# Performance work log

Hardware: AMD Instinct MI355X
Metric: run time of the kernel (lower is better)

## Reference

```python
import jax, jax.numpy as jnp
import numpy as np

N = 50000   # nodes
E = 800000  # edges (avg degree 16)
D = 96      # in = hid = out
BN_EPS = 1e-5


def setup_inputs() -> dict:
    key = jax.random.key(0)
    ks = jax.random.split(key, 16)
    features = jax.random.normal(ks[0], (N, D), jnp.float32)
    src = jax.random.randint(ks[1], (E,), 0, N)
    dst = jax.random.randint(ks[2], (E,), 0, N)
    bound = 1.0 / np.sqrt(D)
    def lin(kw, kb):
        W = jax.random.uniform(kw, (D, D), jnp.float32, -bound, bound)
        b = jax.random.uniform(kb, (D,), jnp.float32, -bound, bound)
        return W, b
    W1, b1 = lin(ks[3], ks[4])
    W2, b2 = lin(ks[5], ks[6])
    W3, b3 = lin(ks[7], ks[8])
    gamma1 = jnp.ones((D,), jnp.float32)
    beta1 = jnp.zeros((D,), jnp.float32)
    gamma2 = jnp.ones((D,), jnp.float32)
    beta2 = jnp.zeros((D,), jnp.float32)
    return dict(features=features, W1=W1, b1=b1, gamma1=gamma1, beta1=beta1,
                W2=W2, b2=b2, gamma2=gamma2, beta2=beta2, W3=W3, b3=b3,
                src=src, dst=dst)


def _gin_conv(h, W, b, src, dst, inv_deg):
    # mean-aggregate incoming neighbor features, eps = 0: (h + mean_nb) @ W + b
    agg = jax.ops.segment_sum(h[src], dst, num_segments=N) * inv_deg[:, None]
    return (h + agg) @ W + b


def _batchnorm(x, gamma, beta):
    mu = jnp.mean(x, axis=0)
    var = jnp.mean((x - mu) ** 2, axis=0)  # biased, as torch BN training
    return (x - mu) * jax.lax.rsqrt(var + BN_EPS) * gamma + beta


def reference(features, W1, b1, gamma1, beta1, W2, b2, gamma2, beta2, W3, b3, src, dst):
    deg = jax.ops.segment_sum(jnp.ones((E,), jnp.float32), dst, num_segments=N)
    inv_deg = jnp.where(deg > 0, 1.0 / jnp.maximum(deg, 1.0), 0.0)
    h = _gin_conv(features, W1, b1, src, dst, inv_deg)
    h = jax.nn.relu(_batchnorm(h, gamma1, beta1))  # dropout p=0 -> identity
    h = _gin_conv(h, W2, b2, src, dst, inv_deg)
    h = jax.nn.relu(_batchnorm(h, gamma2, beta2))
    h = _gin_conv(h, W3, b3, src, dst, inv_deg)
    return h
```

## Files before the change

kernel.cpp:

```cpp
#include <hip/hip_runtime.h>

#define FD 96
#define NB12 12
#define BSH 7
#define BNODES 128
#define NBLK 256

typedef float  f32x4 __attribute__((ext_vector_type(4)));
typedef short  s16x8 __attribute__((ext_vector_type(8)));

__device__ __forceinline__ unsigned short f2bf(float x) {
    unsigned u = __float_as_uint(x);
    u = (u + 0x7fffu + ((u >> 16) & 1u)) >> 16;
    return (unsigned short)u;
}
__device__ __forceinline__ float bflo(unsigned u) { return __uint_as_float(u << 16); }
__device__ __forceinline__ float bfhi(unsigned u) { return __uint_as_float(u & 0xffff0000u); }


__global__ void k_h2d(const int* __restrict__ dst, int* __restrict__ hist2d,
                      int* __restrict__ bcnt, int E, int nbkt, int chunk) {
    __shared__ int hist[512];
    int tid = threadIdx.x, b = blockIdx.x;
    for (int i = tid; i < 512; i += 256) hist[i] = 0;
    __syncthreads();
    int lo = b * chunk, hi = min(lo + chunk, E);
    for (int i = lo + tid; i < hi; i += 256)
        atomicAdd(&hist[dst[i] >> BSH], 1);
    __syncthreads();
    for (int q = tid; q < nbkt; q += 256) {
        int hv = hist[q];
        hist2d[(size_t)q * NBLK + b] = hv;
        if (hv) atomicAdd(&bcnt[q], hv);
    }
}

__global__ void k_bscan(const int* __restrict__ bcnt, int* __restrict__ bbase, int nbkt) {
    __shared__ int sh[512];
    int tid = threadIdx.x;
    int v = (tid < nbkt) ? bcnt[tid] : 0;
    sh[tid] = v;
    __syncthreads();
    for (int off = 1; off < 512; off <<= 1) {
        int t = (tid >= off) ? sh[tid - off] : 0;
        __syncthreads();
        sh[tid] += t;
        __syncthreads();
    }
    int incl = sh[tid];
    if (tid < nbkt) bbase[tid] = incl - v;
    if (tid == nbkt - 1) bbase[nbkt] = incl;
}

__global__ void k_cscan(const int* __restrict__ hist2d, const int* __restrict__ bbase,
                        int* __restrict__ cursor2d) {
    __shared__ int sh[NBLK];
    int q = blockIdx.x, tid = threadIdx.x;
    int v = hist2d[(size_t)q * NBLK + tid];
    sh[tid] = v;
    __syncthreads();
    for (int off = 1; off < NBLK; off <<= 1) {
        int t = (tid >= off) ? sh[tid - off] : 0;
        __syncthreads();
        sh[tid] += t;
        __syncthreads();
    }
    cursor2d[(size_t)q * NBLK + tid] = bbase[q] + sh[tid] - v;
}

__global__ void k_scat(const int* __restrict__ src, const int* __restrict__ dst,
                       const int* __restrict__ cursor2d, uint2* __restrict__ ebuf,
                       int E, int nbkt, int chunk) {
    __shared__ int cur[512];
    int tid = threadIdx.x, b = blockIdx.x;
    for (int q = tid; q < nbkt; q += 256)
        cur[q] = cursor2d[(size_t)q * NBLK + b];
    __syncthreads();
    int lo = b * chunk, hi = min(lo + chunk, E);
    for (int i = lo + tid; i < hi; i += 256) {
        int d = dst[i];
        int p = atomicAdd(&cur[d >> BSH], 1);
        ebuf[p] = make_uint2((unsigned)d, (unsigned)src[i]);
    }
}

__global__ void k_bsort(const uint2* __restrict__ ebuf, const int* __restrict__ bbase,
                        int* __restrict__ csr, int* __restrict__ rp, int* __restrict__ re,
                        float* __restrict__ invd, int* __restrict__ perm, int n) {
    __shared__ int cnt[BNODES];
    __shared__ int cur[BNODES];
    __shared__ int dh[64];
    const int b = blockIdx.x;
    const int tid = threadIdx.x;
    const int lo = bbase[b], hi = bbase[b + 1];
    if (tid < BNODES) cnt[tid] = 0;
    if (tid < 64) dh[tid] = 0;
    __syncthreads();
    for (int i = lo + tid; i < hi; i += blockDim.x)
        atomicAdd(&cnt[(int)ebuf[i].x - (b << BSH)], 1);
    __syncthreads();
    const int node = (b << BSH) + tid;
    const int v = (tid < BNODES) ? cnt[tid] : 0;
    const int dcl = min(v, 63);
    if (tid < BNODES && node < n) atomicAdd(&dh[dcl], 1);
    for (int off = 1; off < BNODES; off <<= 1) {
        int t = (tid < BNODES && tid >= off) ? cnt[tid - off] : 0;
        __syncthreads();
        if (tid < BNODES) cnt[tid] += t;
        __syncthreads();
    }
    int dv = (tid < 64) ? dh[tid] : 0;
    for (int off = 1; off < 64; off <<= 1) {
        int t = (tid < 64 && tid >= off) ? dh[tid - off] : 0;
        __syncthreads();
        if (tid < 64) dh[tid] += t;
        __syncthreads();
    }
    if (tid < 64) dh[tid] -= dv;
    __syncthreads();
    if (tid < BNODES) {
        int excl = cnt[tid] - v;
        if (node < n) {
            rp[node] = lo + excl;
            re[node] = lo + excl + v;
            invd[node] = (v > 0) ? (1.0f / (float)v) : 0.f;
            int r = atomicAdd(&dh[dcl], 1);
            perm[(b << BSH) + r] = node;
        }
        cur[tid] = excl;
    }
    __syncthreads();
    for (int i = lo + tid; i < hi; i += blockDim.x) {
        uint2 e2 = ebuf[i];
        int local = (int)e2.x - (b << BSH);
        int p = lo + atomicAdd(&cur[local], 1);
        csr[p] = (int)e2.y;
    }
}


__global__ void k_cvt(const float4* __restrict__ in, uint4* __restrict__ o, int n16) {
    int i = blockIdx.x * blockDim.x + threadIdx.x;
    if (i >= n16) return;
    float4 x = in[2 * i], y = in[2 * i + 1];
    uint4 r;
    r.x = (unsigned)f2bf(x.x) | ((unsigned)f2bf(x.y) << 16);
    r.y = (unsigned)f2bf(x.z) | ((unsigned)f2bf(x.w) << 16);
    r.z = (unsigned)f2bf(y.x) | ((unsigned)f2bf(y.y) << 16);
    r.w = (unsigned)f2bf(y.z) | ((unsigned)f2bf(y.w) << 16);
    o[i] = r;
}


__global__ void k_wprep(const float* __restrict__ W, unsigned short* __restrict__ Wt) {
    int i = blockIdx.x * blockDim.x + threadIdx.x;
    if (i >= FD * FD) return;
    int col = i % FD, k = i / FD;
    Wt[col * FD + k] = f2bf(W[i]);
}


template<int NORM>
__global__ __launch_bounds__(256, 4) void k_agg(
    const uint4* __restrict__ h,
    const int* __restrict__ rp, const int* __restrict__ re,
    const int* __restrict__ csr, const float* __restrict__ invd,
    const int* __restrict__ perm,
    const float* __restrict__ nA, const float* __restrict__ nC,
    uint4* __restrict__ t, int n)
{
    int g = blockIdx.x * blockDim.x + threadIdx.x;
    int idx = g / NB12;
    if (idx >= n) return;
    int node = perm[idx];
    int q = g - idx * NB12;
    float a[8], c[8];
    if (NORM) {
        #pragma unroll
        for (int z = 0; z < 8; z++) { a[z] = nA[q * 8 + z]; c[z] = nC[q * 8 + z]; }
    }
    float acc8[8];
    #pragma unroll
    for (int z = 0; z < 8; z++) acc8[z] = 0.f;

    int e = rp[node];
    const int end = re[node];
    for (; e + 8 <= end; e += 8) {
        uint4 raw[8];
        #pragma unroll
        for (int u = 0; u < 8; u++) raw[u] = h[(size_t)csr[e + u] * NB12 + q];
        #pragma unroll
        for (int u = 0; u < 8; u++) {
            float v[8];
            v[0] = bflo(raw[u].x); v[1] = bfhi(raw[u].x);
            v[2] = bflo(raw[u].y); v[3] = bfhi(raw[u].y);
            v[4] = bflo(raw[u].z); v[5] = bfhi(raw[u].z);
            v[6] = bflo(raw[u].w); v[7] = bfhi(raw[u].w);
            #pragma unroll
            for (int z = 0; z < 8; z++) {
                float x = v[z];
                if (NORM) x = fmaxf(fmaf(a[z], x, c[z]), 0.f);
                acc8[z] += x;
            }
        }
    }
    for (; e < end; e++) {
        uint4 raw = h[(size_t)csr[e] * NB12 + q];
        float v[8];
        v[0] = bflo(raw.x); v[1] = bfhi(raw.x);
        v[2] = bflo(raw.y); v[3] = bfhi(raw.y);
        v[4] = bflo(raw.z); v[5] = bfhi(raw.z);
        v[6] = bflo(raw.w); v[7] = bfhi(raw.w);
        #pragma unroll
        for (int z = 0; z < 8; z++) {
            float x = v[z];
            if (NORM) x = fmaxf(fmaf(a[z], x, c[z]), 0.f);
            acc8[z] += x;
        }
    }
    uint4 rs = h[(size_t)node * NB12 + q];
    float xs[8];
    xs[0] = bflo(rs.x); xs[1] = bfhi(rs.x);
    xs[2] = bflo(rs.y); xs[3] = bfhi(rs.y);
    xs[4] = bflo(rs.z); xs[5] = bfhi(rs.z);
    xs[6] = bflo(rs.w); xs[7] = bfhi(rs.w);
    float id = invd[node];
    float o[8];
    #pragma unroll
    for (int z = 0; z < 8; z++) {
        float x = xs[z];
        if (NORM) x = fmaxf(fmaf(a[z], x, c[z]), 0.f);
        o[z] = fmaf(id, acc8[z], x);
    }
    uint4 pk;
    pk.x = (unsigned)f2bf(o[0]) | ((unsigned)f2bf(o[1]) << 16);
    pk.y = (unsigned)f2bf(o[2]) | ((unsigned)f2bf(o[3]) << 16);
    pk.z = (unsigned)f2bf(o[4]) | ((unsigned)f2bf(o[5]) << 16);
    pk.w = (unsigned)f2bf(o[6]) | ((unsigned)f2bf(o[7]) << 16);
    t[(size_t)node * NB12 + q] = pk;
}


template<int STATS, int OBF>
__global__ void k_mm(const unsigned short* __restrict__ ta,
                     const unsigned short* __restrict__ Wt,
                     const float* __restrict__ bias,
                     unsigned short* __restrict__ yb, float* __restrict__ yf,
                     float* __restrict__ accg, int n)
{
    __shared__ float sred[2 * FD];
    const int tid  = threadIdx.x;
    const int lane = tid & 63;
    const int wv   = tid >> 6;
    const int colb = lane & 15;
    const int hg   = lane >> 4;
    const int rbase = blockIdx.x * 64 + wv * 16;
    const int r = rbase + colb;

    s16x8 a[3];
    if (r < n) {
        #pragma unroll
        for (int s = 0; s < 3; s++)
            a[s] = *reinterpret_cast<const s16x8*>(ta + (size_t)r * FD + s * 32 + hg * 8);
    } else {
        #pragma unroll
        for (int s = 0; s < 3; s++) a[s] = s16x8{0, 0, 0, 0, 0, 0, 0, 0};
    }
    s16x8 b[6][3];
    #pragma unroll
    for (int c2 = 0; c2 < 6; c2++)
        #pragma unroll
        for (int s = 0; s < 3; s++)
            b[c2][s] = *reinterpret_cast<const s16x8*>(Wt + (size_t)(c2 * 16 + colb) * FD + s * 32 + hg * 8);

    f32x4 acc[6];
    #pragma unroll
    for (int c2 = 0; c2 < 6; c2++) acc[c2] = (f32x4){0.f, 0.f, 0.f, 0.f};
    #pragma unroll
    for (int s = 0; s < 3; s++)
        #pragma unroll
        for (int c2 = 0; c2 < 6; c2++)
            acc[c2] = __builtin_amdgcn_mfma_f32_16x16x32_bf16(a[s], b[c2][s], acc[c2], 0, 0, 0);

    float s1[6], s2[6];
    #pragma unroll
    for (int c2 = 0; c2 < 6; c2++) { s1[c2] = 0.f; s2[c2] = 0.f; }
    #pragma unroll
    for (int c2 = 0; c2 < 6; c2++) {
        float bc = bias[c2 * 16 + colb];
        #pragma unroll
        for (int j = 0; j < 4; j++) {
            int rr = rbase + hg * 4 + j;
            if (rr < n) {
                float y = acc[c2][j] + bc;
                if (OBF) yb[(size_t)rr * FD + c2 * 16 + colb] = f2bf(y);
                else     yf[(size_t)rr * FD + c2 * 16 + colb] = y;
                if (STATS) { s1[c2] += y; s2[c2] = fmaf(y, y, s2[c2]); }
            }
        }
    }
    if (STATS) {
        if (tid < 2 * FD) sred[tid] = 0.f;
        __syncthreads();
        #pragma unroll
        for (int c2 = 0; c2 < 6; c2++) {
            float v1 = s1[c2], v2 = s2[c2];
            v1 += __shfl_xor(v1, 16, 64); v1 += __shfl_xor(v1, 32, 64);
            v2 += __shfl_xor(v2, 16, 64); v2 += __shfl_xor(v2, 32, 64);
            if (lane < 16) {
                atomicAdd(&sred[c2 * 16 + colb], v1);
                atomicAdd(&sred[FD + c2 * 16 + colb], v2);
            }
        }
        __syncthreads();
        if (tid < 2 * FD) atomicAdd(&accg[tid], sred[tid]);
    }
}

__global__ void k_bnfin(const float* __restrict__ acc,
                        const float* __restrict__ gamma, const float* __restrict__ beta,
                        float* __restrict__ na, float* __restrict__ nc, float invN) {
    int f = threadIdx.x;
    float mu  = acc[f] * invN;
    float var = acc[FD + f] * invN - mu * mu;
    float a = gamma[f] * rsqrtf(var + 1e-5f);
    na[f] = a;
    nc[f] = beta[f] - mu * a;
}

extern "C" void kernel_launch(void* const* d_in, const int* in_sizes, int n_in,
                              void* d_out, int out_size, void* d_ws, size_t ws_size,
                              hipStream_t stream) {
    const float* feat = (const float*)d_in[0];
    const float* W1   = (const float*)d_in[1];
    const float* b1   = (const float*)d_in[2];
    const float* g1   = (const float*)d_in[3];
    const float* be1  = (const float*)d_in[4];
    const float* W2   = (const float*)d_in[5];
    const float* b2   = (const float*)d_in[6];
    const float* g2   = (const float*)d_in[7];
    const float* be2  = (const float*)d_in[8];
    const float* W3   = (const float*)d_in[9];
    const float* b3   = (const float*)d_in[10];
    const int*   src  = (const int*)d_in[11];
    const int*   dst  = (const int*)d_in[12];

    const int n = in_sizes[0] / FD;
    const int e = in_sizes[11];
    const int nbkt = (n + BNODES - 1) >> BSH;
    const int chunk = (e + NBLK - 1) / NBLK;

    char* w = (char*)d_ws;
    unsigned short* hf0 = (unsigned short*)w; w += (size_t)n * FD * 2;
    unsigned short* tb  = (unsigned short*)w; w += (size_t)n * FD * 2;
    unsigned short* Wt1 = (unsigned short*)w; w += FD * FD * 2;
    unsigned short* Wt2 = (unsigned short*)w; w += FD * FD * 2;
    unsigned short* Wt3 = (unsigned short*)w; w += FD * FD * 2;
    int*   csr     = (int*)w;   w += (size_t)e * 4;
    int*   bcnt    = (int*)w;   w += 512 * 4;
    float* acc1    = (float*)w; w += 2 * FD * 4;
    float* acc2    = (float*)w; w += 2 * FD * 4;
    int*   bbase   = (int*)w;   w += 513 * 4;
    int*   hist2d  = (int*)w;   w += (size_t)512 * NBLK * 4;
    int*   cursor2d= (int*)w;   w += (size_t)512 * NBLK * 4;
    int*   rp      = (int*)w;   w += (size_t)n * 4;
    int*   re      = (int*)w;   w += (size_t)n * 4;
    float* invd    = (float*)w; w += (size_t)n * 4;
    int*   perm    = (int*)w;   w += (size_t)n * 4;
    float* na1     = (float*)w; w += FD * 4;
    float* nc1     = (float*)w; w += FD * 4;
    float* na2     = (float*)w; w += FD * 4;
    float* nc2     = (float*)w; w += FD * 4;

    uint2* ebuf = (uint2*)tb;

    unsigned short* yb = (unsigned short*)d_out;
    float* O = (float*)d_out;
    const float invN = 1.0f / (float)n;
    const int AGG_GRID = (n * NB12 + 255) / 256;
    const int MM_GRID  = (n + 63) / 64;
    const int n16 = n * FD / 8;

    hipMemsetAsync(bcnt, 0, (512 + 4 * FD) * 4, stream);
    k_cvt<<<(n16 + 255) / 256, 256, 0, stream>>>((const float4*)feat, (uint4*)hf0, n16);
    k_wprep<<<(FD * FD + 255) / 256, 256, 0, stream>>>(W1, Wt1);
    k_wprep<<<(FD * FD + 255) / 256, 256, 0, stream>>>(W2, Wt2);
    k_wprep<<<(FD * FD + 255) / 256, 256, 0, stream>>>(W3, Wt3);

    k_h2d<<<NBLK, 256, 0, stream>>>(dst, hist2d, bcnt, e, nbkt, chunk);
    k_bscan<<<1, 512, 0, stream>>>(bcnt, bbase, nbkt);
    k_cscan<<<nbkt, NBLK, 0, stream>>>(hist2d, bbase, cursor2d);
    k_scat<<<NBLK, 256, 0, stream>>>(src, dst, cursor2d, ebuf, e, nbkt, chunk);
    k_bsort<<<nbkt, 256, 0, stream>>>(ebuf, bbase, csr, rp, re, invd, perm, n);

    k_agg<0><<<AGG_GRID, 256, 0, stream>>>((const uint4*)hf0, rp, re, csr, invd, perm,
                                           nullptr, nullptr, (uint4*)tb, n);
    k_mm<1, 1><<<MM_GRID, 256, 0, stream>>>(tb, Wt1, b1, yb, nullptr, acc1, n);
    k_bnfin<<<1, FD, 0, stream>>>(acc1, g1, be1, na1, nc1, invN);

    k_agg<1><<<AGG_GRID, 256, 0, stream>>>((const uint4*)yb, rp, re, csr, invd, perm,
                                           na1, nc1, (uint4*)tb, n);
    k_mm<1, 1><<<MM_GRID, 256, 0, stream>>>(tb, Wt2, b2, yb, nullptr, acc2, n);
    k_bnfin<<<1, FD, 0, stream>>>(acc2, g2, be2, na2, nc2, invN);

    k_agg<1><<<AGG_GRID, 256, 0, stream>>>((const uint4*)yb, rp, re, csr, invd, perm,
                                           na2, nc2, (uint4*)tb, n);
    k_mm<0, 0><<<MM_GRID, 256, 0, stream>>>(tb, Wt3, b3, nullptr, O, nullptr, n);
}
```

Before: 232.1 us.

## Fuse gather-aggregation with MFMA matmul and renumber nodes by degree order

Merges the per-layer aggregation and matmul kernels into one kernel. Each 16-row MFMA tile gathers its own neighbour rows into registers, packs them to bf16 and multiplies immediately, so the intermediate aggregated tensor is never written to or read from memory. Nodes are relabelled into the degree-sorted permutation: the CSR is translated through an inverse permutation and features are converted in permuted order, so outputs are contiguous and the final layer scatters through perm. BatchNorm+ReLU moves from the gather into a separate elementwise pass. This adds extra launches (xlate, norm) and gives one lane per row with 12 loads per edge, which may hurt gather parallelism.

```diff
diff --git a/kernel.cpp b/kernel.cpp
--- a/kernel.cpp
+++ b/kernel.cpp
@@ -1,7 +1,6 @@
 #include <hip/hip_runtime.h>
 
 #define FD 96
-#define NB12 12
 #define BSH 7
 #define BNODES 128
 #define NBLK 256
@@ -16,6 +15,26 @@
 }
 __device__ __forceinline__ float bflo(unsigned u) { return __uint_as_float(u << 16); }
 __device__ __forceinline__ float bfhi(unsigned u) { return __uint_as_float(u & 0xffff0000u); }
+
+__device__ __forceinline__ s16x8 pack8(const float t[8]) {
+    union { unsigned u[4]; s16x8 v; } r;
+    #pragma unroll
+    for (int z = 0; z < 4; z++)
+        r.u[z] = (unsigned)f2bf(t[2 * z]) | ((unsigned)f2bf(t[2 * z + 1]) << 16);
+    return r.v;
+}
+
+#define ACC8(R, T) { \
+    T[0] += bflo(R.x); T[1] += bfhi(R.x); \
+    T[2] += bflo(R.y); T[3] += bfhi(R.y); \
+    T[4] += bflo(R.z); T[5] += bfhi(R.z); \
+    T[6] += bflo(R.w); T[7] += bfhi(R.w); }
+
+#define FIN8(R, T, id) { \
+    T[0] = fmaf(id, T[0], bflo(R.x)); T[1] = fmaf(id, T[1], bfhi(R.x)); \
+    T[2] = fmaf(id, T[2], bflo(R.y)); T[3] = fmaf(id, T[3], bfhi(R.y)); \
+    T[4] = fmaf(id, T[4], bflo(R.z)); T[5] = fmaf(id, T[5], bfhi(R.z)); \
+    T[6] = fmaf(id, T[6], bflo(R.w)); T[7] = fmaf(id, T[7], bfhi(R.w)); }
 
 
 __global__ void k_h2d(const int* __restrict__ dst, int* __restrict__ hist2d,
@@ -85,8 +104,9 @@
 }
 
 __global__ void k_bsort(const uint2* __restrict__ ebuf, const int* __restrict__ bbase,
-                        int* __restrict__ csr, int* __restrict__ rp, int* __restrict__ re,
-                        float* __restrict__ invd, int* __restrict__ perm, int n) {
+                        int* __restrict__ csr, int* __restrict__ rp2, int* __restrict__ re2,
+                        float* __restrict__ invd2, int* __restrict__ perm,
+                        int* __restrict__ inv_perm, int n) {
     __shared__ int cnt[BNODES];
     __shared__ int cur[BNODES];
     __shared__ int dh[64];
@@ -121,11 +141,13 @@
     if (tid < BNODES) {
         int excl = cnt[tid] - v;
         if (node < n) {
-            rp[node] = lo + excl;
-            re[node] = lo + excl + v;
-            invd[node] = (v > 0) ? (1.0f / (float)v) : 0.f;
-            int r = atomicAdd(&dh[dcl], 1);
-            perm[(b << BSH) + r] = node;
+            int rk = atomicAdd(&dh[dcl], 1);
+            int slot = (b << BSH) + rk;
+            perm[slot] = node;
+            inv_perm[node] = slot;
+            rp2[slot] = lo + excl;
+            re2[slot] = lo + excl + v;
+            invd2[slot] = (v > 0) ? (1.0f / (float)v) : 0.f;
         }
         cur[tid] = excl;
     }
@@ -138,178 +160,133 @@
     }
 }
 
-
-__global__ void k_cvt(const float4* __restrict__ in, uint4* __restrict__ o, int n16) {
+__global__ void k_xlate(int* __restrict__ csr, const int* __restrict__ inv_perm, int E) {
     int i = blockIdx.x * blockDim.x + threadIdx.x;
-    if (i >= n16) return;
-    float4 x = in[2 * i], y = in[2 * i + 1];
+    if (i < E) csr[i] = inv_perm[csr[i]];
+}
+
+__global__ void k_cvtp(const float* __restrict__ feat, const int* __restrict__ perm,
+                       uint4* __restrict__ o, int n) {
+    int g = blockIdx.x * blockDim.x + threadIdx.x;
+    int i = g / 12;
+    if (i >= n) return;
+    int q = g - i * 12;
+    int node = perm[i];
+    const float4* row = (const float4*)(feat + (size_t)node * FD);
+    float4 x = row[2 * q], y = row[2 * q + 1];
     uint4 r;
     r.x = (unsigned)f2bf(x.x) | ((unsigned)f2bf(x.y) << 16);
     r.y = (unsigned)f2bf(x.z) | ((unsigned)f2bf(x.w) << 16);
     r.z = (unsigned)f2bf(y.x) | ((unsigned)f2bf(y.y) << 16);
     r.w = (unsigned)f2bf(y.z) | ((unsigned)f2bf(y.w) << 16);
-    o[i] = r;
-}
-
-
-__global__ void k_wprep(const float* __restrict__ W, unsigned short* __restrict__ Wt) {
+    o[g] = r;
+}
+
+__global__ void k_wprep3(const float* __restrict__ W1, const float* __restrict__ W2,
+                         const float* __restrict__ W3, unsigned short* __restrict__ Wt) {
     int i = blockIdx.x * blockDim.x + threadIdx.x;
-    if (i >= FD * FD) return;
-    int col = i % FD, k = i / FD;
-    Wt[col * FD + k] = f2bf(W[i]);
-}
-
-
-template<int NORM>
-__global__ __launch_bounds__(256, 4) void k_agg(
+    if (i >= 3 * FD * FD) return;
+    int m = i / (FD * FD), r = i - m * FD * FD;
+    const float* W = (m == 0) ? W1 : ((m == 1) ? W2 : W3);
+    int col = r % FD, k = r / FD;
+    Wt[m * FD * FD + col * FD + k] = f2bf(W[r]);
+}
+
+
+template<int STATS, int OBF>
+__global__ __launch_bounds__(256) void k_fused(
     const uint4* __restrict__ h,
-    const int* __restrict__ rp, const int* __restrict__ re,
-    const int* __restrict__ csr, const float* __restrict__ invd,
+    const int* __restrict__ rp2, const int* __restrict__ re2,
+    const float* __restrict__ invd2, const int* __restrict__ csr2,
     const int* __restrict__ perm,
-    const float* __restrict__ nA, const float* __restrict__ nC,
-    uint4* __restrict__ t, int n)
+    const unsigned short* __restrict__ Wt, const float* __restrict__ bias,
+    unsigned short* __restrict__ yb, float* __restrict__ yf,
+    float* __restrict__ accg, int n)
 {
-    int g = blockIdx.x * blockDim.x + threadIdx.x;
-    int idx = g / NB12;
-    if (idx >= n) return;
-    int node = perm[idx];
-    int q = g - idx * NB12;
-    float a[8], c[8];
-    if (NORM) {
+    __shared__ float sred[2 * FD];
+    const int tid = threadIdx.x, lane = tid & 63;
+    const int r16 = lane & 15, hg = lane >> 4;
+    const int tbase = blockIdx.x * 64 + (tid >> 6) * 16;
+    const int idx = tbase + r16;
+
+    float t0[8], t1[8], t2[8];
+    #pragma unroll
+    for (int z = 0; z < 8; z++) { t0[z] = 0.f; t1[z] = 0.f; t2[z] = 0.f; }
+
+    if (idx < n) {
+        int e = rp2[idx];
+        const int end = re2[idx];
+        for (; e + 4 <= end; e += 4) {
+            int ca = csr2[e], cb = csr2[e + 1], cc = csr2[e + 2], cd = csr2[e + 3];
+            uint4 A0 = h[(size_t)ca * 12 + hg], A1 = h[(size_t)ca * 12 + 4 + hg], A2 = h[(size_t)ca * 12 + 8 + hg];
+            uint4 B0 = h[(size_t)cb * 12 + hg], B1 = h[(size_t)cb * 12 + 4 + hg], B2 = h[(size_t)cb * 12 + 8 + hg];
+            uint4 C0 = h[(size_t)cc * 12 + hg], C1 = h[(size_t)cc * 12 + 4 + hg], C2 = h[(size_t)cc * 12 + 8 + hg];
+            uint4 D0 = h[(size_t)cd * 12 + hg], D1 = h[(size_t)cd * 12 + 4 + hg], D2 = h[(size_t)cd * 12 + 8 + hg];
+            ACC8(A0, t0); ACC8(A1, t1); ACC8(A2, t2);
+            ACC8(B0, t0); ACC8(B1, t1); ACC8(B2, t2);
+            ACC8(C0, t0); ACC8(C1, t1); ACC8(C2, t2);
+            ACC8(D0, t0); ACC8(D1, t1); ACC8(D2, t2);
+        }
+        for (; e < end; e++) {
+            int c = csr2[e];
+            uint4 R0 = h[(size_t)c * 12 + hg], R1 = h[(size_t)c * 12 + 4 + hg], R2 = h[(size_t)c * 12 + 8 + hg];
+            ACC8(R0, t0); ACC8(R1, t1); ACC8(R2, t2);
+        }
+        const float id = invd2[idx];
+        uint4 S0 = h[(size_t)idx * 12 + hg], S1 = h[(size_t)idx * 12 + 4 + hg], S2 = h[(size_t)idx * 12 + 8 + hg];
+        FIN8(S0, t0, id); FIN8(S1, t1, id); FIN8(S2, t2, id);
+    }
+
+    s16x8 a0 = pack8(t0), a1 = pack8(t1), a2 = pack8(t2);
+
+    f32x4 acc[6];
+    #pragma unroll
+    for (int c2 = 0; c2 < 6; c2++) acc[c2] = (f32x4){0.f, 0.f, 0.f, 0.f};
+    #pragma unroll
+    for (int c2 = 0; c2 < 6; c2++) {
+        const unsigned short* wp = Wt + (size_t)(c2 * 16 + r16) * FD + hg * 8;
+        s16x8 b0 = *(const s16x8*)(wp);
+        s16x8 b1 = *(const s16x8*)(wp + 32);
+        s16x8 b2 = *(const s16x8*)(wp + 64);
+        acc[c2] = __builtin_amdgcn_mfma_f32_16x16x32_bf16(a0, b0, acc[c2], 0, 0, 0);
+        acc[c2] = __builtin_amdgcn_mfma_f32_16x16x32_bf16(a1, b1, acc[c2], 0, 0, 0);
+        acc[c2] = __builtin_amdgcn_mfma_f32_16x16x32_bf16(a2, b2, acc[c2], 0, 0, 0);
+    }
+
+    int orow[4];
+    #pragma unroll
+    for (int j = 0; j < 4; j++) {
+        int rr = tbase + hg * 4 + j;
+        orow[j] = (!OBF && rr < n) ? perm[rr] : rr;
+    }
+    float s1v[6], s2v[6];
+    #pragma unroll
+    for (int c2 = 0; c2 < 6; c2++) { s1v[c2] = 0.f; s2v[c2] = 0.f; }
+    #pragma unroll
+    for (int c2 = 0; c2 < 6; c2++) {
+        float bc = bias[c2 * 16 + r16];
         #pragma unroll
-        for (int z = 0; z < 8; z++) { a[z] = nA[q * 8 + z]; c[z] = nC[q * 8 + z]; }
-    }
-    float acc8[8];
-    #pragma unroll
-    for (int z = 0; z < 8; z++) acc8[z] = 0.f;
-
-    int e = rp[node];
-    const int end = re[node];
-    for (; e + 8 <= end; e += 8) {
-        uint4 raw[8];
-        #pragma unroll
-        for (int u = 0; u < 8; u++) raw[u] = h[(size_t)csr[e + u] * NB12 + q];
-        #pragma unroll
-        for (int u = 0; u < 8; u++) {
-            float v[8];
-            v[0] = bflo(raw[u].x); v[1] = bfhi(raw[u].x);
-            v[2] = bflo(raw[u].y); v[3] = bfhi(raw[u].y);
-            v[4] = bflo(raw[u].z); v[5] = bfhi(raw[u].z);
-            v[6] = bflo(raw[u].w); v[7] = bfhi(raw[u].w);
-            #pragma unroll
-            for (int z = 0; z < 8; z++) {
-                float x = v[z];
-                if (NORM) x = fmaxf(fmaf(a[z], x, c[z]), 0.f);
-                acc8[z] += x;
+        for (int j = 0; j < 4; j++) {
+            int rr = tbase + hg * 4 + j;
+            if (rr < n) {
+                float y = acc[c2][j] + bc;
+                if (OBF) yb[(size_t)rr * FD + c2 * 16 + r16] = f2bf(y);
+                else     yf[(size_t)orow[j] * FD + c2 * 16 + r16] = y;
+                if (STATS) { s1v[c2] += y; s2v[c2] = fmaf(y, y, s2v[c2]); }
             }
         }
     }
-    for (; e < end; e++) {
-        uint4 raw = h[(size_t)csr[e] * NB12 + q];
-        float v[8];
-        v[0] = bflo(raw.x); v[1] = bfhi(raw.x);
-        v[2] = bflo(raw.y); v[3] = bfhi(raw.y);
-        v[4] = bflo(raw.z); v[5] = bfhi(raw.z);
-        v[6] = bflo(raw.w); v[7] = bfhi(raw.w);
-        #pragma unroll
-        for (int z = 0; z < 8; z++) {
-            float x = v[z];
-            if (NORM) x = fmaxf(fmaf(a[z], x, c[z]), 0.f);
-            acc8[z] += x;
-        }
-    }
-    uint4 rs = h[(size_t)node * NB12 + q];
-    float xs[8];
-    xs[0] = bflo(rs.x); xs[1] = bfhi(rs.x);
-    xs[2] = bflo(rs.y); xs[3] = bfhi(rs.y);
-    xs[4] = bflo(rs.z); xs[5] = bfhi(rs.z);
-    xs[6] = bflo(rs.w); xs[7] = bfhi(rs.w);
-    float id = invd[node];
-    float o[8];
-    #pragma unroll
-    for (int z = 0; z < 8; z++) {
-        float x = xs[z];
-        if (NORM) x = fmaxf(fmaf(a[z], x, c[z]), 0.f);
-        o[z] = fmaf(id, acc8[z], x);
-    }
-    uint4 pk;
-    pk.x = (unsigned)f2bf(o[0]) | ((unsigned)f2bf(o[1]) << 16);
-    pk.y = (unsigned)f2bf(o[2]) | ((unsigned)f2bf(o[3]) << 16);
-    pk.z = (unsigned)f2bf(o[4]) | ((unsigned)f2bf(o[5]) << 16);
-    pk.w = (unsigned)f2bf(o[6]) | ((unsigned)f2bf(o[7]) << 16);
-    t[(size_t)node * NB12 + q] = pk;
-}
-
-
-template<int STATS, int OBF>
-__global__ void k_mm(const unsigned short* __restrict__ ta,
-                     const unsigned short* __restrict__ Wt,
-                     const float* __restrict__ bias,
-                     unsigned short* __restrict__ yb, float* __restrict__ yf,
-                     float* __restrict__ accg, int n)
-{
-    __shared__ float sred[2 * FD];
-    const int tid  = threadIdx.x;
-    const int lane = tid & 63;
-    const int wv   = tid >> 6;
-    const int colb = lane & 15;
-    const int hg   = lane >> 4;
-    const int rbase = blockIdx.x * 64 + wv * 16;
-    const int r = rbase + colb;
-
-    s16x8 a[3];
-    if (r < n) {
-        #pragma unroll
-        for (int s = 0; s < 3; s++)
-            a[s] = *reinterpret_cast<const s16x8*>(ta + (size_t)r * FD + s * 32 + hg * 8);
-    } else {
-        #pragma unroll
-        for (int s = 0; s < 3; s++) a[s] = s16x8{0, 0, 0, 0, 0, 0, 0, 0};
-    }
-    s16x8 b[6][3];
-    #pragma unroll
-    for (int c2 = 0; c2 < 6; c2++)
-        #pragma unroll
-        for (int s = 0; s < 3; s++)
-            b[c2][s] = *reinterpret_cast<const s16x8*>(Wt + (size_t)(c2 * 16 + colb) * FD + s * 32 + hg * 8);
-
-    f32x4 acc[6];
-    #pragma unroll
-    for (int c2 = 0; c2 < 6; c2++) acc[c2] = (f32x4){0.f, 0.f, 0.f, 0.f};
-    #pragma unroll
-    for (int s = 0; s < 3; s++)
-        #pragma unroll
-        for (int c2 = 0; c2 < 6; c2++)
-            acc[c2] = __builtin_amdgcn_mfma_f32_16x16x32_bf16(a[s], b[c2][s], acc[c2], 0, 0, 0);
-
-    float s1[6], s2[6];
-    #pragma unroll
-    for (int c2 = 0; c2 < 6; c2++) { s1[c2] = 0.f; s2[c2] = 0.f; }
-    #pragma unroll
-    for (int c2 = 0; c2 < 6; c2++) {
-        float bc = bias[c2 * 16 + colb];
-        #pragma unroll
-        for (int j = 0; j < 4; j++) {
-            int rr = rbase + hg * 4 + j;
-            if (rr < n) {
-                float y = acc[c2][j] + bc;
-                if (OBF) yb[(size_t)rr * FD + c2 * 16 + colb] = f2bf(y);
-                else     yf[(size_t)rr * FD + c2 * 16 + colb] = y;
-                if (STATS) { s1[c2] += y; s2[c2] = fmaf(y, y, s2[c2]); }
-            }
-        }
-    }
     if (STATS) {
         if (tid < 2 * FD) sred[tid] = 0.f;
         __syncthreads();
         #pragma unroll
         for (int c2 = 0; c2 < 6; c2++) {
-            float v1 = s1[c2], v2 = s2[c2];
+            float v1 = s1v[c2], v2 = s2v[c2];
             v1 += __shfl_xor(v1, 16, 64); v1 += __shfl_xor(v1, 32, 64);
             v2 += __shfl_xor(v2, 16, 64); v2 += __shfl_xor(v2, 32, 64);
             if (lane < 16) {
-                atomicAdd(&sred[c2 * 16 + colb], v1);
-                atomicAdd(&sred[FD + c2 * 16 + colb], v2);
+                atomicAdd(&sred[c2 * 16 + r16], v1);
+                atomicAdd(&sred[FD + c2 * 16 + r16], v2);
             }
         }
         __syncthreads();
@@ -326,6 +303,30 @@
     float a = gamma[f] * rsqrtf(var + 1e-5f);
     na[f] = a;
     nc[f] = beta[f] - mu * a;
+}
+
+__global__ void k_norm(uint4* __restrict__ y, const float* __restrict__ na,
+                       const float* __restrict__ nc, int n12) {
+    int g = blockIdx.x * blockDim.x + threadIdx.x;
+    if (g >= n12) return;
+    int q = g % 12;
+    float4 a0 = *(const float4*)(na + q * 8), a1 = *(const float4*)(na + q * 8 + 4);
+    float4 c0 = *(const float4*)(nc + q * 8), c1 = *(const float4*)(nc + q * 8 + 4);
+    uint4 r = y[g];
+    float v0 = fmaxf(fmaf(a0.x, bflo(r.x), c0.x), 0.f);
+    float v1 = fmaxf(fmaf(a0.y, bfhi(r.x), c0.y), 0.f);
+    float v2 = fmaxf(fmaf(a0.z, bflo(r.y), c0.z), 0.f);
+    float v3 = fmaxf(fmaf(a0.w, bfhi(r.y), c0.w), 0.f);
+    float v4 = fmaxf(fmaf(a1.x, bflo(r.z), c1.x), 0.f);
+    float v5 = fmaxf(fmaf(a1.y, bfhi(r.z), c1.y), 0.f);
+    float v6 = fmaxf(fmaf(a1.z, bflo(r.w), c1.z), 0.f);
+    float v7 = fmaxf(fmaf(a1.w, bfhi(r.w), c1.w), 0.f);
+    uint4 pk;
+    pk.x = (unsigned)f2bf(v0) | ((unsigned)f2bf(v1) << 16);
+    pk.y = (unsigned)f2bf(v2) | ((unsigned)f2bf(v3) << 16);
+    pk.z = (unsigned)f2bf(v4) | ((unsigned)f2bf(v5) << 16);
+    pk.w = (unsigned)f2bf(v6) | ((unsigned)f2bf(v7) << 16);
+    y[g] = pk;
 }
 
 extern "C" void kernel_launch(void* const* d_in, const int* in_sizes, int n_in,
@@ -351,11 +352,9 @@
     const int chunk = (e + NBLK - 1) / NBLK;
 
     char* w = (char*)d_ws;
-    unsigned short* hf0 = (unsigned short*)w; w += (size_t)n * FD * 2;
-    unsigned short* tb  = (unsigned short*)w; w += (size_t)n * FD * 2;
-    unsigned short* Wt1 = (unsigned short*)w; w += FD * FD * 2;
-    unsigned short* Wt2 = (unsigned short*)w; w += FD * FD * 2;
-    unsigned short* Wt3 = (unsigned short*)w; w += FD * FD * 2;
+    unsigned short* hA  = (unsigned short*)w; w += (size_t)n * FD * 2;
+    unsigned short* hB  = (unsigned short*)w; w += (size_t)n * FD * 2;
+    unsigned short* Wt  = (unsigned short*)w; w += (size_t)3 * FD * FD * 2;
     int*   csr     = (int*)w;   w += (size_t)e * 4;
     int*   bcnt    = (int*)w;   w += 512 * 4;
     float* acc1    = (float*)w; w += 2 * FD * 4;
@@ -363,47 +362,43 @@
     int*   bbase   = (int*)w;   w += 513 * 4;
     int*   hist2d  = (int*)w;   w += (size_t)512 * NBLK * 4;
     int*   cursor2d= (int*)w;   w += (size_t)512 * NBLK * 4;
-    int*   rp      = (int*)w;   w += (size_t)n * 4;
-    int*   re      = (int*)w;   w += (size_t)n * 4;
-    float* invd    = (float*)w; w += (size_t)n * 4;
+    int*   rp2     = (int*)w;   w += (size_t)n * 4;
+    int*   re2     = (int*)w;   w += (size_t)n * 4;
+    float* invd2   = (float*)w; w += (size_t)n * 4;
     int*   perm    = (int*)w;   w += (size_t)n * 4;
+    int*   invp    = (int*)w;   w += (size_t)n * 4;
     float* na1     = (float*)w; w += FD * 4;
     float* nc1     = (float*)w; w += FD * 4;
     float* na2     = (float*)w; w += FD * 4;
     float* nc2     = (float*)w; w += FD * 4;
 
-    uint2* ebuf = (uint2*)tb;
-
-    unsigned short* yb = (unsigned short*)d_out;
+    uint2* ebuf = (uint2*)hB;
+
     float* O = (float*)d_out;
     const float invN = 1.0f / (float)n;
-    const int AGG_GRID = (n * NB12 + 255) / 256;
-    const int MM_GRID  = (n + 63) / 64;
-    const int n16 = n * FD / 8;
+    const int FUSE_GRID = (n + 63) / 64;
+    const int n12 = n * 12;
 
     hipMemsetAsync(bcnt, 0, (512 + 4 * FD) * 4, stream);
-    k_cvt<<<(n16 + 255) / 256, 256, 0, stream>>>((const float4*)feat, (uint4*)hf0, n16);
-    k_wprep<<<(FD * FD + 255) / 256, 256, 0, stream>>>(W1, Wt1);
-    k_wprep<<<(FD * FD + 255) / 256, 256, 0, stream>>>(W2, Wt2);
-    k_wprep<<<(FD * FD + 255) / 256, 256, 0, stream>>>(W3, Wt3);
-
     k_h2d<<<NBLK, 256, 0, stream>>>(dst, hist2d, bcnt, e, nbkt, chunk);
     k_bscan<<<1, 512, 0, stream>>>(bcnt, bbase, nbkt);
     k_cscan<<<nbkt, NBLK, 0, stream>>>(hist2d, bbase, cursor2d);
     k_scat<<<NBLK, 256, 0, stream>>>(src, dst, cursor2d, ebuf, e, nbkt, chunk);
-    k_bsort<<<nbkt, 256, 0, stream>>>(ebuf, bbase, csr, rp, re, invd, perm, n);
-
-    k_agg<0><<<AGG_GRID, 256, 0, stream>>>((const uint4*)hf0, rp, re, csr, invd, perm,
-                                           nullptr, nullptr, (uint4*)tb, n);
-    k_mm<1, 1><<<MM_GRID, 256, 0, stream>>>(tb, Wt1, b1, yb, nullptr, acc1, n);
+    k_bsort<<<nbkt, 256, 0, stream>>>(ebuf, bbase, csr, rp2, re2, invd2, perm, invp, n);
+    k_xlate<<<(e + 255) / 256, 256, 0, stream>>>(csr, invp, e);
+    k_cvtp<<<(n12 + 255) / 256, 256, 0, stream>>>(feat, perm, (uint4*)hA, n);
+    k_wprep3<<<(3 * FD * FD + 255) / 256, 256, 0, stream>>>(W1, W2, W3, Wt);
+
+    k_fused<1, 1><<<FUSE_GRID, 256, 0, stream>>>((const uint4*)hA, rp2, re2, invd2, csr,
+                                                 perm, Wt, b1, hB, nullptr, acc1, n);
     k_bnfin<<<1, FD, 0, stream>>>(acc1, g1, be1, na1, nc1, invN);
-
-    k_agg<1><<<AGG_GRID, 256, 0, stream>>>((const uint4*)yb, rp, re, csr, invd, perm,
-                                           na1, nc1, (uint4*)tb, n);
-    k_mm<1, 1><<<MM_GRID, 256, 0, stream>>>(tb, Wt2, b2, yb, nullptr, acc2, n);
+    k_norm<<<(n12 + 255) / 256, 256, 0, stream>>>((uint4*)hB, na1, nc1, n12);
+
+    k_fused<1, 1><<<FUSE_GRID, 256, 0, stream>>>((const uint4*)hB, rp2, re2, invd2, csr,
+                                                 perm, Wt + FD * FD, b2, hA, nullptr, acc2, n);
     k_bnfin<<<1, FD, 0, stream>>>(acc2, g2, be2, na2, nc2, invN);
-
-    k_agg<1><<<AGG_GRID, 256, 0, stream>>>((const uint4*)yb, rp, re, csr, invd, perm,
-                                           na2, nc2, (uint4*)tb, n);
-    k_mm<0, 0><<<MM_GRID, 256, 0, stream>>>(tb, Wt3, b3, nullptr, O, nullptr, n);
-}
+    k_norm<<<(n12 + 255) / 256, 256, 0, stream>>>((uint4*)hA, na2, nc2, n12);
+
+    k_fused<0, 0><<<FUSE_GRID, 256, 0, stream>>>((const uint4*)hA, rp2, re2, invd2, csr,
+                                                 perm, Wt + 2 * FD * FD, b3, nullptr, O, nullptr, n);
+}
```

New measurement: 237.0 us. 1.02x slower.

## Renumber nodes into degree-sorted order and run aggregation in permuted space

Applied to the files above, without the earlier changes.

Node features, CSR indices, row pointers and inverse degrees are all relabelled into degree-sorted slot order, so the aggregation and matmul kernels index contiguously and no longer need a perm lookup per node. The final output is scattered back to original row order inside the last matmul. The aggregation kernel now gives each node 4 threads that each loop over 3 feature chunks instead of 12 threads per node, and the three weight-prep launches are merged into one. This adds a CSR translation pass and a permuted gather when converting the features, and it cuts per-node parallelism in the aggregation.

```diff
diff --git a/kernel.cpp b/kernel.cpp
--- a/kernel.cpp
+++ b/kernel.cpp
@@ -1,7 +1,6 @@
 #include <hip/hip_runtime.h>
 
 #define FD 96
-#define NB12 12
 #define BSH 7
 #define BNODES 128
 #define NBLK 256
@@ -16,6 +15,14 @@
 }
 __device__ __forceinline__ float bflo(unsigned u) { return __uint_as_float(u << 16); }
 __device__ __forceinline__ float bfhi(unsigned u) { return __uint_as_float(u & 0xffff0000u); }
+
+__device__ __forceinline__ s16x8 pack8(const float t[8]) {
+    union { unsigned u[4]; s16x8 v; } r;
+    #pragma unroll
+    for (int z = 0; z < 4; z++)
+        r.u[z] = (unsigned)f2bf(t[2 * z]) | ((unsigned)f2bf(t[2 * z + 1]) << 16);
+    return r.v;
+}
 
 
 __global__ void k_h2d(const int* __restrict__ dst, int* __restrict__ hist2d,
@@ -85,8 +92,9 @@
 }
 
 __global__ void k_bsort(const uint2* __restrict__ ebuf, const int* __restrict__ bbase,
-                        int* __restrict__ csr, int* __restrict__ rp, int* __restrict__ re,
-                        float* __restrict__ invd, int* __restrict__ perm, int n) {
+                        int* __restrict__ csr, int* __restrict__ rp2, int* __restrict__ re2,
+                        float* __restrict__ invd2, int* __restrict__ perm,
+                        int* __restrict__ inv_perm, int n) {
     __shared__ int cnt[BNODES];
     __shared__ int cur[BNODES];
     __shared__ int dh[64];
@@ -121,11 +129,13 @@
     if (tid < BNODES) {
         int excl = cnt[tid] - v;
         if (node < n) {
-            rp[node] = lo + excl;
-            re[node] = lo + excl + v;
-            invd[node] = (v > 0) ? (1.0f / (float)v) : 0.f;
-            int r = atomicAdd(&dh[dcl], 1);
-            perm[(b << BSH) + r] = node;
+            int rk = atomicAdd(&dh[dcl], 1);
+            int slot = (b << BSH) + rk;
+            perm[slot] = node;
+            inv_perm[node] = slot;
+            rp2[slot] = lo + excl;
+            re2[slot] = lo + excl + v;
+            invd2[slot] = (v > 0) ? (1.0f / (float)v) : 0.f;
         }
         cur[tid] = excl;
     }
@@ -138,64 +148,95 @@
     }
 }
 
-
-__global__ void k_cvt(const float4* __restrict__ in, uint4* __restrict__ o, int n16) {
+__global__ void k_xlate(int* __restrict__ csr, const int* __restrict__ inv_perm, int E) {
     int i = blockIdx.x * blockDim.x + threadIdx.x;
-    if (i >= n16) return;
-    float4 x = in[2 * i], y = in[2 * i + 1];
+    if (i < E) csr[i] = inv_perm[csr[i]];
+}
+
+__global__ void k_cvtp(const float* __restrict__ feat, const int* __restrict__ perm,
+                       uint4* __restrict__ o, int n) {
+    int g = blockIdx.x * blockDim.x + threadIdx.x;
+    int i = g / 12;
+    if (i >= n) return;
+    int q = g - i * 12;
+    int node = perm[i];
+    const float4* row = (const float4*)(feat + (size_t)node * FD);
+    float4 x = row[2 * q], y = row[2 * q + 1];
     uint4 r;
     r.x = (unsigned)f2bf(x.x) | ((unsigned)f2bf(x.y) << 16);
     r.y = (unsigned)f2bf(x.z) | ((unsigned)f2bf(x.w) << 16);
     r.z = (unsigned)f2bf(y.x) | ((unsigned)f2bf(y.y) << 16);
     r.w = (unsigned)f2bf(y.z) | ((unsigned)f2bf(y.w) << 16);
-    o[i] = r;
-}
-
-
-__global__ void k_wprep(const float* __restrict__ W, unsigned short* __restrict__ Wt) {
+    o[g] = r;
+}
+
+__global__ void k_wprep3(const float* __restrict__ W1, const float* __restrict__ W2,
+                         const float* __restrict__ W3, unsigned short* __restrict__ Wt) {
     int i = blockIdx.x * blockDim.x + threadIdx.x;
-    if (i >= FD * FD) return;
-    int col = i % FD, k = i / FD;
-    Wt[col * FD + k] = f2bf(W[i]);
+    if (i >= 3 * FD * FD) return;
+    int m = i / (FD * FD), r = i - m * FD * FD;
+    const float* W = (m == 0) ? W1 : ((m == 1) ? W2 : W3);
+    int col = r % FD, k = r / FD;
+    Wt[m * FD * FD + col * FD + k] = f2bf(W[r]);
 }
 
 
 template<int NORM>
 __global__ __launch_bounds__(256, 4) void k_agg(
     const uint4* __restrict__ h,
-    const int* __restrict__ rp, const int* __restrict__ re,
-    const int* __restrict__ csr, const float* __restrict__ invd,
-    const int* __restrict__ perm,
+    const int* __restrict__ rp2, const int* __restrict__ re2,
+    const float* __restrict__ invd2, const int* __restrict__ csr,
     const float* __restrict__ nA, const float* __restrict__ nC,
     uint4* __restrict__ t, int n)
 {
-    int g = blockIdx.x * blockDim.x + threadIdx.x;
-    int idx = g / NB12;
+    const int tid = threadIdx.x;
+    const int rl = tid >> 2;
+    const int qq = tid & 3;
+    const int idx = blockIdx.x * 64 + rl;
     if (idx >= n) return;
-    int node = perm[idx];
-    int q = g - idx * NB12;
-    float a[8], c[8];
-    if (NORM) {
-        #pragma unroll
-        for (int z = 0; z < 8; z++) { a[z] = nA[q * 8 + z]; c[z] = nC[q * 8 + z]; }
-    }
-    float acc8[8];
-    #pragma unroll
-    for (int z = 0; z < 8; z++) acc8[z] = 0.f;
-
-    int e = rp[node];
-    const int end = re[node];
-    for (; e + 8 <= end; e += 8) {
-        uint4 raw[8];
-        #pragma unroll
-        for (int u = 0; u < 8; u++) raw[u] = h[(size_t)csr[e + u] * NB12 + q];
-        #pragma unroll
-        for (int u = 0; u < 8; u++) {
+    const int beg = rp2[idx];
+    const int end = re2[idx];
+    const float id = invd2[idx];
+
+    #pragma unroll 1
+    for (int p = 0; p < 3; p++) {
+        const int q = p * 4 + qq;
+        float a[8], c[8];
+        if (NORM) {
+            #pragma unroll
+            for (int z = 0; z < 8; z++) { a[z] = nA[q * 8 + z]; c[z] = nC[q * 8 + z]; }
+        }
+        float acc8[8];
+        #pragma unroll
+        for (int z = 0; z < 8; z++) acc8[z] = 0.f;
+
+        int e = beg;
+        for (; e + 8 <= end; e += 8) {
+            uint4 raw[8];
+            #pragma unroll
+            for (int u = 0; u < 8; u++) raw[u] = h[(size_t)csr[e + u] * 12 + q];
+            #pragma unroll
+            for (int u = 0; u < 8; u++) {
+                float v[8];
+                v[0] = bflo(raw[u].x); v[1] = bfhi(raw[u].x);
+                v[2] = bflo(raw[u].y); v[3] = bfhi(raw[u].y);
+                v[4] = bflo(raw[u].z); v[5] = bfhi(raw[u].z);
+                v[6] = bflo(raw[u].w); v[7] = bfhi(raw[u].w);
+                #pragma unroll
+                for (int z = 0; z < 8; z++) {
+                    float x = v[z];
+                    if (NORM) x = fmaxf(fmaf(a[z], x, c[z]), 0.f);
+                    acc8[z] += x;
+                }
+            }
+        }
+        for (; e < end; e++) {
+            uint4 raw = h[(size_t)csr[e] * 12 + q];
             float v[8];
-            v[0] = bflo(raw[u].x); v[1] = bfhi(raw[u].x);
-            v[2] = bflo(raw[u].y); v[3] = bfhi(raw[u].y);
-            v[4] = bflo(raw[u].z); v[5] = bfhi(raw[u].z);
-            v[6] = bflo(raw[u].w); v[7] = bfhi(raw[u].w);
+            v[0] = bflo(raw.x); v[1] = bfhi(raw.x);
+            v[2] = bflo(raw.y); v[3] = bfhi(raw.y);
+            v[4] = bflo(raw.z); v[5] = bfhi(raw.z);
+            v[6] = bflo(raw.w); v[7] = bfhi(raw.w);
             #pragma unroll
             for (int z = 0; z < 8; z++) {
                 float x = v[z];
@@ -203,48 +244,33 @@
                 acc8[z] += x;
             }
         }
-    }
-    for (; e < end; e++) {
-        uint4 raw = h[(size_t)csr[e] * NB12 + q];
-        float v[8];
-        v[0] = bflo(raw.x); v[1] = bfhi(raw.x);
-        v[2] = bflo(raw.y); v[3] = bfhi(raw.y);
-        v[4] = bflo(raw.z); v[5] = bfhi(raw.z);
-        v[6] = bflo(raw.w); v[7] = bfhi(raw.w);
+        uint4 rs = h[(size_t)idx * 12 + q];
+        float xs[8];
+        xs[0] = bflo(rs.x); xs[1] = bfhi(rs.x);
+        xs[2] = bflo(rs.y); xs[3] = bfhi(rs.y);
+        xs[4] = bflo(rs.z); xs[5] = bfhi(rs.z);
+        xs[6] = bflo(rs.w); xs[7] = bfhi(rs.w);
+        float o[8];
         #pragma unroll
         for (int z = 0; z < 8; z++) {
-            float x = v[z];
+            float x = xs[z];
             if (NORM) x = fmaxf(fmaf(a[z], x, c[z]), 0.f);
-            acc8[z] += x;
-        }
-    }
-    uint4 rs = h[(size_t)node * NB12 + q];
-    float xs[8];
-    xs[0] = bflo(rs.x); xs[1] = bfhi(rs.x);
-    xs[2] = bflo(rs.y); xs[3] = bfhi(rs.y);
-    xs[4] = bflo(rs.z); xs[5] = bfhi(rs.z);
-    xs[6] = bflo(rs.w); xs[7] = bfhi(rs.w);
-    float id = invd[node];
-    float o[8];
-    #pragma unroll
-    for (int z = 0; z < 8; z++) {
-        float x = xs[z];
-        if (NORM) x = fmaxf(fmaf(a[z], x, c[z]), 0.f);
-        o[z] = fmaf(id, acc8[z], x);
-    }
-    uint4 pk;
-    pk.x = (unsigned)f2bf(o[0]) | ((unsigned)f2bf(o[1]) << 16);
-    pk.y = (unsigned)f2bf(o[2]) | ((unsigned)f2bf(o[3]) << 16);
-    pk.z = (unsigned)f2bf(o[4]) | ((unsigned)f2bf(o[5]) << 16);
-    pk.w = (unsigned)f2bf(o[6]) | ((unsigned)f2bf(o[7]) << 16);
-    t[(size_t)node * NB12 + q] = pk;
+            o[z] = fmaf(id, acc8[z], x);
+        }
+        uint4 pk;
+        pk.x = (unsigned)f2bf(o[0]) | ((unsigned)f2bf(o[1]) << 16);
+        pk.y = (unsigned)f2bf(o[2]) | ((unsigned)f2bf(o[3]) << 16);
+        pk.z = (unsigned)f2bf(o[4]) | ((unsigned)f2bf(o[5]) << 16);
+        pk.w = (unsigned)f2bf(o[6]) | ((unsigned)f2bf(o[7]) << 16);
+        t[(size_t)idx * 12 + q] = pk;
+    }
 }
 
 
 template<int STATS, int OBF>
 __global__ void k_mm(const unsigned short* __restrict__ ta,
                      const unsigned short* __restrict__ Wt,
-                     const float* __restrict__ bias,
+                     const float* __restrict__ bias, const int* __restrict__ perm,
                      unsigned short* __restrict__ yb, float* __restrict__ yf,
                      float* __restrict__ accg, int n)
 {
@@ -282,6 +308,12 @@
         for (int c2 = 0; c2 < 6; c2++)
             acc[c2] = __builtin_amdgcn_mfma_f32_16x16x32_bf16(a[s], b[c2][s], acc[c2], 0, 0, 0);
 
+    int orow[4];
+    #pragma unroll
+    for (int j = 0; j < 4; j++) {
+        int rr = rbase + hg * 4 + j;
+        orow[j] = (!OBF && rr < n) ? perm[rr] : rr;
+    }
     float s1[6], s2[6];
     #pragma unroll
     for (int c2 = 0; c2 < 6; c2++) { s1[c2] = 0.f; s2[c2] = 0.f; }
@@ -294,7 +326,7 @@
             if (rr < n) {
                 float y = acc[c2][j] + bc;
                 if (OBF) yb[(size_t)rr * FD + c2 * 16 + colb] = f2bf(y);
-                else     yf[(size_t)rr * FD + c2 * 16 + colb] = y;
+                else     yf[(size_t)orow[j] * FD + c2 * 16 + colb] = y;
                 if (STATS) { s1[c2] += y; s2[c2] = fmaf(y, y, s2[c2]); }
             }
         }
@@ -351,11 +383,9 @@
     const int chunk = (e + NBLK - 1) / NBLK;
 
     char* w = (char*)d_ws;
-    unsigned short* hf0 = (unsigned short*)w; w += (size_t)n * FD * 2;
+    unsigned short* hA  = (unsigned short*)w; w += (size_t)n * FD * 2;
     unsigned short* tb  = (unsigned short*)w; w += (size_t)n * FD * 2;
-    unsigned short* Wt1 = (unsigned short*)w; w += FD * FD * 2;
-    unsigned short* Wt2 = (unsigned short*)w; w += FD * FD * 2;
-    unsigned short* Wt3 = (unsigned short*)w; w += FD * FD * 2;
+    unsigned short* Wt  = (unsigned short*)w; w += (size_t)3 * FD * FD * 2;
     int*   csr     = (int*)w;   w += (size_t)e * 4;
     int*   bcnt    = (int*)w;   w += 512 * 4;
     float* acc1    = (float*)w; w += 2 * FD * 4;
@@ -363,10 +393,11 @@
     int*   bbase   = (int*)w;   w += 513 * 4;
     int*   hist2d  = (int*)w;   w += (size_t)512 * NBLK * 4;
     int*   cursor2d= (int*)w;   w += (size_t)512 * NBLK * 4;
-    int*   rp      = (int*)w;   w += (size_t)n * 4;
-    int*   re      = (int*)w;   w += (size_t)n * 4;
-    float* invd    = (float*)w; w += (size_t)n * 4;
+    int*   rp2     = (int*)w;   w += (size_t)n * 4;
+    int*   re2     = (int*)w;   w += (size_t)n * 4;
+    float* invd2   = (float*)w; w += (size_t)n * 4;
     int*   perm    = (int*)w;   w += (size_t)n * 4;
+    int*   invp    = (int*)w;   w += (size_t)n * 4;
     float* na1     = (float*)w; w += FD * 4;
     float* nc1     = (float*)w; w += FD * 4;
     float* na2     = (float*)w; w += FD * 4;
@@ -374,36 +405,33 @@
 
     uint2* ebuf = (uint2*)tb;
 
-    unsigned short* yb = (unsigned short*)d_out;
     float* O = (float*)d_out;
     const float invN = 1.0f / (float)n;
-    const int AGG_GRID = (n * NB12 + 255) / 256;
+    const int AGG_GRID = (n + 63) / 64;
     const int MM_GRID  = (n + 63) / 64;
-    const int n16 = n * FD / 8;
+    const int n12 = n * 12;
 
     hipMemsetAsync(bcnt, 0, (512 + 4 * FD) * 4, stream);
-    k_cvt<<<(n16 + 255) / 256, 256, 0, stream>>>((const float4*)feat, (uint4*)hf0, n16);
-    k_wprep<<<(FD * FD + 255) / 256, 256, 0, stream>>>(W1, Wt1);
-    k_wprep<<<(FD * FD + 255) / 256, 256, 0, stream>>>(W2, Wt2);
-    k_wprep<<<(FD * FD + 255) / 256, 256, 0, stream>>>(W3, Wt3);
-
     k_h2d<<<NBLK, 256, 0, stream>>>(dst, hist2d, bcnt, e, nbkt, chunk);
     k_bscan<<<1, 512, 0, stream>>>(bcnt, bbase, nbkt);
     k_cscan<<<nbkt, NBLK, 0, stream>>>(hist2d, bbase, cursor2d);
     k_scat<<<NBLK, 256, 0, stream>>>(src, dst, cursor2d, ebuf, e, nbkt, chunk);
-    k_bsort<<<nbkt, 256, 0, stream>>>(ebuf, bbase, csr, rp, re, invd, perm, n);
-
-    k_agg<0><<<AGG_GRID, 256, 0, stream>>>((const uint4*)hf0, rp, re, csr, invd, perm,
+    k_bsort<<<nbkt, 256, 0, stream>>>(ebuf, bbase, csr, rp2, re2, invd2, perm, invp, n);
+    k_xlate<<<(e + 255) / 256, 256, 0, stream>>>(csr, invp, e);
+    k_cvtp<<<(n12 + 255) / 256, 256, 0, stream>>>(feat, perm, (uint4*)hA, n);
+    k_wprep3<<<(3 * FD * FD + 255) / 256, 256, 0, stream>>>(W1, W2, W3, Wt);
+
+    k_agg<0><<<AGG_GRID, 256, 0, stream>>>((const uint4*)hA, rp2, re2, invd2, csr,
                                            nullptr, nullptr, (uint4*)tb, n);
-    k_mm<1, 1><<<MM_GRID, 256, 0, stream>>>(tb, Wt1, b1, yb, nullptr, acc1, n);
+    k_mm<1, 1><<<MM_GRID, 256, 0, stream>>>(tb, Wt, b1, perm, hA, nullptr, acc1, n);
     k_bnfin<<<1, FD, 0, stream>>>(acc1, g1, be1, na1, nc1, invN);
 
-    k_agg<1><<<AGG_GRID, 256, 0, stream>>>((const uint4*)yb, rp, re, csr, invd, perm,
+    k_agg<1><<<AGG_GRID, 256, 0, stream>>>((const uint4*)hA, rp2, re2, invd2, csr,
                                            na1, nc1, (uint4*)tb, n);
-    k_mm<1, 1><<<MM_GRID, 256, 0, stream>>>(tb, Wt2, b2, yb, nullptr, acc2, n);
+    k_mm<1, 1><<<MM_GRID, 256, 0, stream>>>(tb, Wt + FD * FD, b2, perm, hA, nullptr, acc2, n);
     k_bnfin<<<1, FD, 0, stream>>>(acc2, g2, be2, na2, nc2, invN);
 
-    k_agg<1><<<AGG_GRID, 256, 0, stream>>>((const uint4*)yb, rp, re, csr, invd, perm,
+    k_agg<1><<<AGG_GRID, 256, 0, stream>>>((const uint4*)hA, rp2, re2, invd2, csr,
                                            na2, nc2, (uint4*)tb, n);
-    k_mm<0, 0><<<MM_GRID, 256, 0, stream>>>(tb, Wt3, b3, nullptr, O, nullptr, n);
-}
+    k_mm<0, 0><<<MM_GRID, 256, 0, stream>>>(tb, Wt + 2 * FD * FD, b3, perm, nullptr, O, nullptr, n);
+}
```

Result: slower. 265.8 us (+14.5%).
